# Performance work log

Hardware: AMD Instinct MI355X
Metric: run time of the kernel (lower is better)

Reference implementation:

```python
import jax, jax.numpy as jnp
import numpy as np

IN_DIM = 128
OUT_DIM = 128
NUM_HEADS = 4
HEAD_DIM = OUT_DIM // NUM_HEADS  # 32
B, N = 4, 4096


def setup_inputs() -> dict:
    key = jax.random.key(0)
    ks = jax.random.split(key, 7)
    s_in = 1.0 / np.sqrt(IN_DIM)
    s_out = 1.0 / np.sqrt(OUT_DIM)
    return {
        "x": jax.random.normal(ks[0], (B, N, IN_DIM), dtype=jnp.float32),
        "adjacency": jax.random.randint(ks[1], (N, N), 0, 2, dtype=jnp.int32),
        "W_q": jax.random.uniform(ks[2], (IN_DIM, NUM_HEADS * HEAD_DIM), jnp.float32, -s_in, s_in),
        "W_k": jax.random.uniform(ks[3], (IN_DIM, NUM_HEADS * HEAD_DIM), jnp.float32, -s_in, s_in),
        "W_v": jax.random.uniform(ks[4], (IN_DIM, NUM_HEADS * HEAD_DIM), jnp.float32, -s_in, s_in),
        "W_o": jax.random.uniform(ks[5], (OUT_DIM, OUT_DIM), jnp.float32, -s_out, s_out),
        "b_o": jax.random.uniform(ks[6], (OUT_DIM,), jnp.float32, -s_out, s_out),
    }


def reference(x, adjacency, W_q, W_k, W_v, W_o, b_o):
    Bn, Nn, _ = x.shape
    # QKV projections -> (B, H, N, Dh)
    q = (x @ W_q).reshape(Bn, Nn, NUM_HEADS, HEAD_DIM).transpose(0, 2, 1, 3)
    k = (x @ W_k).reshape(Bn, Nn, NUM_HEADS, HEAD_DIM).transpose(0, 2, 1, 3)
    v = (x @ W_v).reshape(Bn, Nn, NUM_HEADS, HEAD_DIM).transpose(0, 2, 1, 3)
    scores = jnp.einsum("bhnd,bhmd->bhnm", q, k) / np.sqrt(HEAD_DIM).astype(np.float32)
    # adjacency mask (1,1,N,N): -inf where no edge
    adj = adjacency[None, None, :, :]
    scores = jnp.where(adj == 0, -jnp.inf, scores)
    attn = jax.nn.softmax(scores, axis=-1)
    out = jnp.einsum("bhnm,bhmd->bhnd", attn, v)
    out = out.transpose(0, 2, 1, 3).reshape(Bn, Nn, NUM_HEADS * HEAD_DIM)  # concat heads
    return out @ W_o + b_o
```

## Files before the change

### kernel.cpp

```cpp
#include <hip/hip_runtime.h>
#include <stdint.h>

typedef __attribute__((ext_vector_type(4))) short short4v;
typedef __attribute__((ext_vector_type(8))) short bf16x8;
typedef __attribute__((ext_vector_type(4))) float f32x4;
typedef __attribute__((ext_vector_type(2))) uint32_t uint2v;
typedef __attribute__((ext_vector_type(4))) uint32_t uint4v;
typedef __attribute__((ext_vector_type(4))) uint16_t ushort4v;

#define NN 4096

__device__ __forceinline__ uint16_t f2bf(float f) {
    union { float f; uint32_t u; } c; c.f = f;
    uint32_t r = c.u + 0x7FFF + ((c.u >> 16) & 1);
    return (uint16_t)(r >> 16);
}

__global__ __launch_bounds__(256) void pack_kernel(
    const int* __restrict__ adj, uint64_t* __restrict__ bits,
    const float* __restrict__ Wq, const float* __restrict__ Wk,
    const float* __restrict__ Wv, const float* __restrict__ Wo,
    uint16_t* __restrict__ WT, uint16_t* __restrict__ WoT)
{
    const int lane = threadIdx.x & 63;
    const int wave = (blockIdx.x * blockDim.x + threadIdx.x) >> 6;
    const int nwaves = (gridDim.x * blockDim.x) >> 6;
    const int TOT = (NN * NN) / 64;
    for (int i = wave; i < TOT; i += nwaves) {
        int v = adj[(size_t)i * 64 + lane];
        uint64_t m = __ballot(v != 0);
        if (lane == 0) bits[i] = m;
    }
    const int tid = blockIdx.x * blockDim.x + threadIdx.x;
    const int nth = gridDim.x * blockDim.x;
    for (int t = tid; t < 3 * 128 * 128 + 128 * 128; t += nth) {
        if (t < 3 * 128 * 128) {
            int j = t >> 7, k = t & 127;
            int m = j >> 7, jj = j & 127;
            const float* W = (m == 0) ? Wq : ((m == 1) ? Wk : Wv);
            float v = W[k * 128 + jj];
            if (m == 0) v *= (0.17677669529663687f * 1.4426950408889634f);
            WT[t] = f2bf(v);
        } else {
            int t2 = t - 3 * 128 * 128;
            int j = t2 >> 7, k = t2 & 127;
            WoT[t2] = f2bf(Wo[k * 128 + j]);
        }
    }
}

__global__ __launch_bounds__(256) void qkv_kernel(
    const float* __restrict__ x, const uint16_t* __restrict__ WT,
    uint16_t* __restrict__ Q, uint16_t* __restrict__ Kf, uint16_t* __restrict__ Vf)
{
    const int wave = threadIdx.x >> 6, lane = threadIdx.x & 63;
    const int g = lane >> 4, l15 = lane & 15;
    const int ntile = blockIdx.x * 4 + wave;
    const int n = ntile * 16 + l15;
    const int b = n >> 12, nn = n & 4095;

    const char* xrow = (const char*)x + (size_t)n * 512;
    bf16x8 xb[4];
#pragma unroll
    for (int ks = 0; ks < 4; ++ks) {
        f32x4 a = *(const f32x4*)(xrow + ks * 128 + g * 16);
        f32x4 c = *(const f32x4*)(xrow + ks * 128 + 64 + g * 16);
        bf16x8 f;
#pragma unroll
        for (int i = 0; i < 4; ++i) { f[i] = (short)f2bf(a[i]); f[4 + i] = (short)f2bf(c[i]); }
        xb[ks] = f;
    }

#pragma unroll 1
    for (int jt = 0; jt < 24; ++jt) {
        const int j0 = jt * 16;
        const bool isV = (j0 >= 256);
        const char* wrow = (const char*)WT + (size_t)(j0 + l15) * 256;
        f32x4 acc = {0.f, 0.f, 0.f, 0.f};
#pragma unroll
        for (int ks = 0; ks < 4; ++ks) {
            short4v a0 = *(const short4v*)(wrow + ks * 64 + g * 8);
            short4v a1 = *(const short4v*)(wrow + ks * 64 + 32 + g * 8);
            bf16x8 af = __builtin_shufflevector(a0, a1, 0, 1, 2, 3, 4, 5, 6, 7);
            acc = isV ? __builtin_amdgcn_mfma_f32_16x16x32_bf16(xb[ks], af, acc, 0, 0, 0)
                      : __builtin_amdgcn_mfma_f32_16x16x32_bf16(af, xb[ks], acc, 0, 0, 0);
        }
        const int m = j0 >> 7;
        const int bh = b * 4 + ((j0 & 127) >> 5);
        const int half = (j0 >> 4) & 1;
        ushort4v st;
#pragma unroll
        for (int r = 0; r < 4; ++r) st[r] = f2bf(acc[r]);
        if (m == 0) {
            const int d0 = (j0 & 31) + g * 4;
            *(ushort4v*)(Q + ((size_t)bh * 4096 + nn) * 32 + d0) = st;
        } else if (m == 1) {
            *(ushort4v*)(Kf + ((size_t)bh << 17) + (ntile & 255) * 512 + lane * 8 + half * 4) = st;
        } else {
            *(ushort4v*)(Vf + ((size_t)bh << 17) + ((ntile & 255) >> 1) * 1024
                         + half * 512 + lane * 8 + ((ntile & 1) << 2)) = st;
        }
    }
}

__global__ __launch_bounds__(512, 2) void attn_kernel(
    const uint16_t* __restrict__ Q, const uint16_t* __restrict__ Kf,
    const uint16_t* __restrict__ Vf, const uint32_t* __restrict__ bits,
    uint16_t* __restrict__ O)
{
    __shared__ f32x4 cmb[4][4][2][64];
    __shared__ float csum[4][4][64];
    const int tid = threadIdx.x;
    const int wave = tid >> 6, lane = tid & 63;
    const int g = lane >> 4, l15 = lane & 15, gsh = g * 4;
    const int blk = blockIdx.x;
    const int bh = ((blk & 7) << 1) | ((blk >> 3) & 1);
    const int qb = blk >> 4;
    const int q0 = qb * 64;

    const char* Kp = (const char*)Kf + ((size_t)bh << 18) + wave * 32768 + lane * 16;
    const char* Vp = (const char*)Vf + ((size_t)bh << 18) + wave * 32768 + lane * 16;
    const uint32_t* ap[4];
#pragma unroll
    for (int qg = 0; qg < 4; ++qg)
        ap[qg] = bits + (size_t)(q0 + qg * 16 + l15) * 128 + wave * 16;

    bf16x8 qf[4];
#pragma unroll
    for (int qg = 0; qg < 4; ++qg) {
        const char* qrow = (const char*)Q + ((size_t)bh * 4096 + q0 + qg * 16 + l15) * 64;
        short4v a0 = *(const short4v*)(qrow + g * 8);
        short4v a1 = *(const short4v*)(qrow + 32 + g * 8);
        qf[qg] = __builtin_shufflevector(a0, a1, 0, 1, 2, 3, 4, 5, 6, 7);
    }

    bf16x8 ones;
#pragma unroll
    for (int i = 0; i < 8; ++i) ones[i] = (short)0x3F80;

    const f32x4 z = {0.f, 0.f, 0.f, 0.f};
    f32x4 o[4][2], sacc[4];
#pragma unroll
    for (int qg = 0; qg < 4; ++qg) { o[qg][0] = z; o[qg][1] = z; sacc[qg] = z; }

#pragma unroll 1
    for (int t = 0; t < 8; ++t) {
        bf16x8 kc[4], vc[4];
#pragma unroll
        for (int j = 0; j < 4; ++j) kc[j] = *(const bf16x8*)(Kp + j * 1024);
#pragma unroll
        for (int i = 0; i < 4; ++i) vc[i] = *(const bf16x8*)(Vp + i * 1024);
        Kp += 4096; Vp += 4096;
        uint2v wc[4];
#pragma unroll
        for (int qg = 0; qg < 4; ++qg) { wc[qg] = *(const uint2v*)ap[qg]; ap[qg] += 2; }

#pragma unroll
        for (int qg = 0; qg < 4; ++qg) {
            f32x4 s[4];
#pragma unroll
            for (int j = 0; j < 4; ++j)
                s[j] = __builtin_amdgcn_mfma_f32_16x16x32_bf16(kc[j], qf[qg], z, 0, 0, 0);
            float p[16];
#pragma unroll
            for (int j = 0; j < 4; ++j) {
                uint32_t wj = wc[qg][j >> 1] >> (((j & 1) << 4) + gsh);
#pragma unroll
                for (int r = 0; r < 4; ++r) {
                    float pv = __builtin_amdgcn_exp2f(s[j][r]);
                    int msk = ((int)(wj << (31 - r))) >> 31;
                    p[j * 4 + r] = __uint_as_float(__float_as_uint(pv) & (uint32_t)msk);
                }
            }
            uint32_t pk[8];
#pragma unroll
            for (int i = 0; i < 8; ++i) {
                uint32_t r_;
                asm("v_cvt_pk_bf16_f32 %0, %1, %2" : "=v"(r_) : "v"(p[2 * i]), "v"(p[2 * i + 1]));
                pk[i] = r_;
            }
            uint4v u0 = {pk[0], pk[1], pk[2], pk[3]};
            uint4v u1 = {pk[4], pk[5], pk[6], pk[7]};
            bf16x8 pf0 = __builtin_bit_cast(bf16x8, u0);
            bf16x8 pf1 = __builtin_bit_cast(bf16x8, u1);
            o[qg][0] = __builtin_amdgcn_mfma_f32_16x16x32_bf16(vc[0], pf0, o[qg][0], 0, 0, 0);
            o[qg][0] = __builtin_amdgcn_mfma_f32_16x16x32_bf16(vc[2], pf1, o[qg][0], 0, 0, 0);
            o[qg][1] = __builtin_amdgcn_mfma_f32_16x16x32_bf16(vc[1], pf0, o[qg][1], 0, 0, 0);
            o[qg][1] = __builtin_amdgcn_mfma_f32_16x16x32_bf16(vc[3], pf1, o[qg][1], 0, 0, 0);
            sacc[qg] = __builtin_amdgcn_mfma_f32_16x16x32_bf16(ones, pf0, sacc[qg], 0, 0, 0);
            sacc[qg] = __builtin_amdgcn_mfma_f32_16x16x32_bf16(ones, pf1, sacc[qg], 0, 0, 0);
        }
    }

    if (wave < 4) {
#pragma unroll
        for (int qg = 0; qg < 4; ++qg) {
            cmb[wave][qg][0][lane] = o[qg][0];
            cmb[wave][qg][1][lane] = o[qg][1];
            csum[wave][qg][lane] = sacc[qg][0];
        }
    }
    __syncthreads();
    if (wave >= 4) {
        const int w2 = wave - 4;
#pragma unroll
        for (int qg = 0; qg < 4; ++qg) {
            cmb[w2][qg][0][lane] += o[qg][0];
            cmb[w2][qg][1][lane] += o[qg][1];
            csum[w2][qg][lane] += sacc[qg][0];
        }
    }
    __syncthreads();
    {
        const int qg = wave & 3, h = wave >> 2;
        f32x4 a = cmb[0][qg][h][lane] + cmb[1][qg][h][lane]
                + cmb[2][qg][h][lane] + cmb[3][qg][h][lane];
        float sd = csum[0][qg][lane] + csum[1][qg][lane]
                 + csum[2][qg][lane] + csum[3][qg][lane];
        const float inv = 1.0f / sd;
        const int q = q0 + qg * 16 + l15;
        uint16_t* orow = O + ((size_t)bh * 4096 + q) * 32;
        ushort4v st;
#pragma unroll
        for (int r = 0; r < 4; ++r) st[r] = f2bf(a[r] * inv);
        *(ushort4v*)(orow + h * 16 + gsh) = st;
    }
}

__global__ __launch_bounds__(256) void proj_kernel(
    const uint16_t* __restrict__ A, const uint16_t* __restrict__ WoT,
    const float* __restrict__ bo, float* __restrict__ out)
{
    const int wave = threadIdx.x >> 6, lane = threadIdx.x & 63;
    const int g = lane >> 4, l15 = lane & 15;
    const int ntile = blockIdx.x * 4 + wave;
    const int n = ntile * 16 + l15;
    const int b = n >> 12, nn = n & 4095;

    bf16x8 bfr[4];
#pragma unroll
    for (int h = 0; h < 4; ++h) {
        const char* arow = (const char*)A + (((size_t)(b * 4 + h)) * 4096 + nn) * 64;
        short4v a0 = *(const short4v*)(arow + g * 8);
        short4v a1 = *(const short4v*)(arow + 32 + g * 8);
        bfr[h] = __builtin_shufflevector(a0, a1, 0, 1, 2, 3, 4, 5, 6, 7);
    }
#pragma unroll 1
    for (int ct = 0; ct < 8; ++ct) {
        const int c0 = ct * 16;
        const char* wrow = (const char*)WoT + (size_t)(c0 + l15) * 256;
        f32x4 acc = {0.f, 0.f, 0.f, 0.f};
#pragma unroll
        for (int h = 0; h < 4; ++h) {
            short4v a0 = *(const short4v*)(wrow + h * 64 + g * 8);
            short4v a1 = *(const short4v*)(wrow + h * 64 + 32 + g * 8);
            bf16x8 af = __builtin_shufflevector(a0, a1, 0, 1, 2, 3, 4, 5, 6, 7);
            acc = __builtin_amdgcn_mfma_f32_16x16x32_bf16(af, bfr[h], acc, 0, 0, 0);
        }
        f32x4 bias = *(const f32x4*)(bo + c0 + g * 4);
#pragma unroll
        for (int r = 0; r < 4; ++r) acc[r] += bias[r];
        *(f32x4*)(out + (size_t)n * 128 + c0 + g * 4) = acc;
    }
}

extern "C" void kernel_launch(void* const* d_in, const int* in_sizes, int n_in,
                              void* d_out, int out_size, void* d_ws, size_t ws_size,
                              hipStream_t stream)
{
    const float* x   = (const float*)d_in[0];
    const int*   adj = (const int*)d_in[1];
    const float* Wq  = (const float*)d_in[2];
    const float* Wk  = (const float*)d_in[3];
    const float* Wv  = (const float*)d_in[4];
    const float* Wo  = (const float*)d_in[5];
    const float* bo  = (const float*)d_in[6];
    float* out = (float*)d_out;

    char* ws = (char*)d_ws;
    uint16_t* Q    = (uint16_t*)(ws);
    uint16_t* Kf   = (uint16_t*)(ws + ((size_t)4 << 20));
    uint16_t* Vf   = (uint16_t*)(ws + ((size_t)8 << 20));
    uint16_t* AO   = (uint16_t*)(ws + ((size_t)12 << 20));
    uint32_t* bits = (uint32_t*)(ws + ((size_t)16 << 20));
    uint16_t* WT   = (uint16_t*)(ws + ((size_t)18 << 20));
    uint16_t* WoT  = (uint16_t*)(ws + ((size_t)18 << 20) + 98304);

    hipLaunchKernelGGL(pack_kernel, dim3(2048), dim3(256), 0, stream,
                       adj, (uint64_t*)bits, Wq, Wk, Wv, Wo, WT, WoT);
    hipLaunchKernelGGL(qkv_kernel, dim3(256), dim3(256), 0, stream,
                       x, WT, Q, Kf, Vf);
    hipLaunchKernelGGL(attn_kernel, dim3(1024), dim3(512), 0, stream,
                       Q, Kf, Vf, bits, AO);
    hipLaunchKernelGGL(proj_kernel, dim3(256), dim3(256), 0, stream,
                       AO, WoT, bo, out);
}
```

Baseline: 133.2 us.

## Rebalance kernels: split weight pack, overlap adjacency packing with QKV, retile attention

New measurement: 130.1 us. -2.3%, faster.

```diff
diff --git a/kernel.cpp b/kernel.cpp
--- a/kernel.cpp
+++ b/kernel.cpp
@@ -16,46 +16,50 @@
     return (uint16_t)(r >> 16);
 }
 
-__global__ __launch_bounds__(256) void pack_kernel(
-    const int* __restrict__ adj, uint64_t* __restrict__ bits,
+__global__ __launch_bounds__(256) void wpack_kernel(
     const float* __restrict__ Wq, const float* __restrict__ Wk,
     const float* __restrict__ Wv, const float* __restrict__ Wo,
     uint16_t* __restrict__ WT, uint16_t* __restrict__ WoT)
 {
-    const int lane = threadIdx.x & 63;
-    const int wave = (blockIdx.x * blockDim.x + threadIdx.x) >> 6;
-    const int nwaves = (gridDim.x * blockDim.x) >> 6;
-    const int TOT = (NN * NN) / 64;
-    for (int i = wave; i < TOT; i += nwaves) {
-        int v = adj[(size_t)i * 64 + lane];
-        uint64_t m = __ballot(v != 0);
-        if (lane == 0) bits[i] = m;
-    }
-    const int tid = blockIdx.x * blockDim.x + threadIdx.x;
-    const int nth = gridDim.x * blockDim.x;
-    for (int t = tid; t < 3 * 128 * 128 + 128 * 128; t += nth) {
-        if (t < 3 * 128 * 128) {
-            int j = t >> 7, k = t & 127;
-            int m = j >> 7, jj = j & 127;
-            const float* W = (m == 0) ? Wq : ((m == 1) ? Wk : Wv);
-            float v = W[k * 128 + jj];
-            if (m == 0) v *= (0.17677669529663687f * 1.4426950408889634f);
-            WT[t] = f2bf(v);
-        } else {
-            int t2 = t - 3 * 128 * 128;
-            int j = t2 >> 7, k = t2 & 127;
-            WoT[t2] = f2bf(Wo[k * 128 + j]);
-        }
-    }
-}
-
-__global__ __launch_bounds__(256) void qkv_kernel(
+    const int t = blockIdx.x * 256 + threadIdx.x;
+    if (t < 3 * 128 * 128) {
+        int j = t >> 7, k = t & 127;
+        int m = j >> 7, jj = j & 127;
+        const float* W = (m == 0) ? Wq : ((m == 1) ? Wk : Wv);
+        float v = W[k * 128 + jj];
+        if (m == 0) v *= (0.17677669529663687f * 1.4426950408889634f);
+        WT[t] = f2bf(v);
+    } else {
+        int t2 = t - 3 * 128 * 128;
+        int j = t2 >> 7, k = t2 & 127;
+        WoT[t2] = f2bf(Wo[k * 128 + j]);
+    }
+}
+
+__global__ __launch_bounds__(256) void adjqkv_kernel(
+    const int* __restrict__ adj, uint64_t* __restrict__ bits,
     const float* __restrict__ x, const uint16_t* __restrict__ WT,
     uint16_t* __restrict__ Q, uint16_t* __restrict__ Kf, uint16_t* __restrict__ Vf)
 {
-    const int wave = threadIdx.x >> 6, lane = threadIdx.x & 63;
+    const int blk = blockIdx.x;
+    const int tid = threadIdx.x;
+    const int wave = tid >> 6, lane = tid & 63;
+
+    if (blk >= 768) {
+        const int ablk = blk - 768;
+        const int wid = (ablk * 256 + tid) >> 6;
+        const int TOT = (NN * NN) / 64;
+        for (int i = wid; i < TOT; i += 8192) {
+            int v = adj[(size_t)i * 64 + lane];
+            uint64_t m = __ballot(v != 0);
+            if (lane == 0) bits[i] = m;
+        }
+        return;
+    }
+
     const int g = lane >> 4, l15 = lane & 15;
-    const int ntile = blockIdx.x * 4 + wave;
+    const int m = blk >> 8;
+    const int ntile = (blk & 255) * 4 + wave;
     const int n = ntile * 16 + l15;
     const int b = n >> 12, nn = n & 4095;
 
@@ -72,9 +76,9 @@
     }
 
 #pragma unroll 1
-    for (int jt = 0; jt < 24; ++jt) {
+    for (int jt = m * 8; jt < m * 8 + 8; ++jt) {
         const int j0 = jt * 16;
-        const bool isV = (j0 >= 256);
+        const bool isV = (m == 2);
         const char* wrow = (const char*)WT + (size_t)(j0 + l15) * 256;
         f32x4 acc = {0.f, 0.f, 0.f, 0.f};
 #pragma unroll
@@ -85,7 +89,6 @@
             acc = isV ? __builtin_amdgcn_mfma_f32_16x16x32_bf16(xb[ks], af, acc, 0, 0, 0)
                       : __builtin_amdgcn_mfma_f32_16x16x32_bf16(af, xb[ks], acc, 0, 0, 0);
         }
-        const int m = j0 >> 7;
         const int bh = b * 4 + ((j0 & 127) >> 5);
         const int half = (j0 >> 4) & 1;
         ushort4v st;
@@ -103,31 +106,29 @@
     }
 }
 
-__global__ __launch_bounds__(512, 2) void attn_kernel(
+__global__ __launch_bounds__(256) void attn_kernel(
     const uint16_t* __restrict__ Q, const uint16_t* __restrict__ Kf,
     const uint16_t* __restrict__ Vf, const uint32_t* __restrict__ bits,
     uint16_t* __restrict__ O)
 {
-    __shared__ f32x4 cmb[4][4][2][64];
-    __shared__ float csum[4][4][64];
+    __shared__ f32x4 cmb[4][2][2][64];
+    __shared__ float csum[4][2][64];
     const int tid = threadIdx.x;
     const int wave = tid >> 6, lane = tid & 63;
     const int g = lane >> 4, l15 = lane & 15, gsh = g * 4;
     const int blk = blockIdx.x;
     const int bh = ((blk & 7) << 1) | ((blk >> 3) & 1);
     const int qb = blk >> 4;
-    const int q0 = qb * 64;
-
-    const char* Kp = (const char*)Kf + ((size_t)bh << 18) + wave * 32768 + lane * 16;
-    const char* Vp = (const char*)Vf + ((size_t)bh << 18) + wave * 32768 + lane * 16;
-    const uint32_t* ap[4];
-#pragma unroll
-    for (int qg = 0; qg < 4; ++qg)
-        ap[qg] = bits + (size_t)(q0 + qg * 16 + l15) * 128 + wave * 16;
-
-    bf16x8 qf[4];
-#pragma unroll
-    for (int qg = 0; qg < 4; ++qg) {
+    const int q0 = qb * 32;
+
+    const char* Kp = (const char*)Kf + ((size_t)bh << 18) + wave * 65536 + lane * 16;
+    const char* Vp = (const char*)Vf + ((size_t)bh << 18) + wave * 65536 + lane * 16;
+    const uint32_t* ap0 = bits + (size_t)(q0 + l15) * 128 + wave * 32;
+    const uint32_t* ap1 = bits + (size_t)(q0 + 16 + l15) * 128 + wave * 32;
+
+    bf16x8 qf[2];
+#pragma unroll
+    for (int qg = 0; qg < 2; ++qg) {
         const char* qrow = (const char*)Q + ((size_t)bh * 4096 + q0 + qg * 16 + l15) * 64;
         short4v a0 = *(const short4v*)(qrow + g * 8);
         short4v a1 = *(const short4v*)(qrow + 32 + g * 8);
@@ -139,80 +140,65 @@
     for (int i = 0; i < 8; ++i) ones[i] = (short)0x3F80;
 
     const f32x4 z = {0.f, 0.f, 0.f, 0.f};
-    f32x4 o[4][2], sacc[4];
-#pragma unroll
-    for (int qg = 0; qg < 4; ++qg) { o[qg][0] = z; o[qg][1] = z; sacc[qg] = z; }
+    f32x4 o[2][2], sacc[2];
+#pragma unroll
+    for (int qg = 0; qg < 2; ++qg) { o[qg][0] = z; o[qg][1] = z; sacc[qg] = z; }
 
 #pragma unroll 1
-    for (int t = 0; t < 8; ++t) {
+    for (int t = 0; t < 16; ++t) {
         bf16x8 kc[4], vc[4];
 #pragma unroll
         for (int j = 0; j < 4; ++j) kc[j] = *(const bf16x8*)(Kp + j * 1024);
 #pragma unroll
         for (int i = 0; i < 4; ++i) vc[i] = *(const bf16x8*)(Vp + i * 1024);
         Kp += 4096; Vp += 4096;
-        uint2v wc[4];
-#pragma unroll
-        for (int qg = 0; qg < 4; ++qg) { wc[qg] = *(const uint2v*)ap[qg]; ap[qg] += 2; }
-
-#pragma unroll
-        for (int qg = 0; qg < 4; ++qg) {
-            f32x4 s[4];
-#pragma unroll
-            for (int j = 0; j < 4; ++j)
-                s[j] = __builtin_amdgcn_mfma_f32_16x16x32_bf16(kc[j], qf[qg], z, 0, 0, 0);
-            float p[16];
-#pragma unroll
-            for (int j = 0; j < 4; ++j) {
-                uint32_t wj = wc[qg][j >> 1] >> (((j & 1) << 4) + gsh);
+        uint2v wc0 = *(const uint2v*)ap0;  ap0 += 2;
+        uint2v wc1 = *(const uint2v*)ap1;  ap1 += 2;
+
+#pragma unroll
+        for (int qg = 0; qg < 2; ++qg) {
+            const uint2v wc = qg ? wc1 : wc0;
+#pragma unroll
+            for (int half32 = 0; half32 < 2; ++half32) {
+                f32x4 s0 = __builtin_amdgcn_mfma_f32_16x16x32_bf16(kc[half32 * 2], qf[qg], z, 0, 0, 0);
+                f32x4 s1 = __builtin_amdgcn_mfma_f32_16x16x32_bf16(kc[half32 * 2 + 1], qf[qg], z, 0, 0, 0);
+                uint32_t wlo = (wc[half32]) >> gsh;
+                uint32_t whi = (wc[half32]) >> (16 + gsh);
+                float p[8];
 #pragma unroll
                 for (int r = 0; r < 4; ++r) {
-                    float pv = __builtin_amdgcn_exp2f(s[j][r]);
-                    int msk = ((int)(wj << (31 - r))) >> 31;
-                    p[j * 4 + r] = __uint_as_float(__float_as_uint(pv) & (uint32_t)msk);
+                    float pv0 = __builtin_amdgcn_exp2f(s0[r]);
+                    int m0 = ((int)(wlo << (31 - r))) >> 31;
+                    p[r] = __uint_as_float(__float_as_uint(pv0) & (uint32_t)m0);
+                    float pv1 = __builtin_amdgcn_exp2f(s1[r]);
+                    int m1 = ((int)(whi << (31 - r))) >> 31;
+                    p[4 + r] = __uint_as_float(__float_as_uint(pv1) & (uint32_t)m1);
                 }
+                uint32_t pk[4];
+#pragma unroll
+                for (int i = 0; i < 4; ++i) {
+                    uint32_t r_;
+                    asm("v_cvt_pk_bf16_f32 %0, %1, %2" : "=v"(r_) : "v"(p[2 * i]), "v"(p[2 * i + 1]));
+                    pk[i] = r_;
+                }
+                uint4v u = {pk[0], pk[1], pk[2], pk[3]};
+                bf16x8 pf = __builtin_bit_cast(bf16x8, u);
+                o[qg][0] = __builtin_amdgcn_mfma_f32_16x16x32_bf16(vc[half32 * 2], pf, o[qg][0], 0, 0, 0);
+                o[qg][1] = __builtin_amdgcn_mfma_f32_16x16x32_bf16(vc[half32 * 2 + 1], pf, o[qg][1], 0, 0, 0);
+                sacc[qg] = __builtin_amdgcn_mfma_f32_16x16x32_bf16(ones, pf, sacc[qg], 0, 0, 0);
             }
-            uint32_t pk[8];
-#pragma unroll
-            for (int i = 0; i < 8; ++i) {
-                uint32_t r_;
-                asm("v_cvt_pk_bf16_f32 %0, %1, %2" : "=v"(r_) : "v"(p[2 * i]), "v"(p[2 * i + 1]));
-                pk[i] = r_;
-            }
-            uint4v u0 = {pk[0], pk[1], pk[2], pk[3]};
-            uint4v u1 = {pk[4], pk[5], pk[6], pk[7]};
-            bf16x8 pf0 = __builtin_bit_cast(bf16x8, u0);
-            bf16x8 pf1 = __builtin_bit_cast(bf16x8, u1);
-            o[qg][0] = __builtin_amdgcn_mfma_f32_16x16x32_bf16(vc[0], pf0, o[qg][0], 0, 0, 0);
-            o[qg][0] = __builtin_amdgcn_mfma_f32_16x16x32_bf16(vc[2], pf1, o[qg][0], 0, 0, 0);
-            o[qg][1] = __builtin_amdgcn_mfma_f32_16x16x32_bf16(vc[1], pf0, o[qg][1], 0, 0, 0);
-            o[qg][1] = __builtin_amdgcn_mfma_f32_16x16x32_bf16(vc[3], pf1, o[qg][1], 0, 0, 0);
-            sacc[qg] = __builtin_amdgcn_mfma_f32_16x16x32_bf16(ones, pf0, sacc[qg], 0, 0, 0);
-            sacc[qg] = __builtin_amdgcn_mfma_f32_16x16x32_bf16(ones, pf1, sacc[qg], 0, 0, 0);
-        }
-    }
-
-    if (wave < 4) {
-#pragma unroll
-        for (int qg = 0; qg < 4; ++qg) {
-            cmb[wave][qg][0][lane] = o[qg][0];
-            cmb[wave][qg][1][lane] = o[qg][1];
-            csum[wave][qg][lane] = sacc[qg][0];
-        }
-    }
-    __syncthreads();
-    if (wave >= 4) {
-        const int w2 = wave - 4;
-#pragma unroll
-        for (int qg = 0; qg < 4; ++qg) {
-            cmb[w2][qg][0][lane] += o[qg][0];
-            cmb[w2][qg][1][lane] += o[qg][1];
-            csum[w2][qg][lane] += sacc[qg][0];
-        }
+        }
+    }
+
+#pragma unroll
+    for (int qg = 0; qg < 2; ++qg) {
+        cmb[wave][qg][0][lane] = o[qg][0];
+        cmb[wave][qg][1][lane] = o[qg][1];
+        csum[wave][qg][lane] = sacc[qg][0];
     }
     __syncthreads();
     {
-        const int qg = wave & 3, h = wave >> 2;
+        const int qg = wave >> 1, h = wave & 1;
         f32x4 a = cmb[0][qg][h][lane] + cmb[1][qg][h][lane]
                 + cmb[2][qg][h][lane] + cmb[3][qg][h][lane];
         float sd = csum[0][qg][lane] + csum[1][qg][lane]
@@ -233,7 +219,9 @@
 {
     const int wave = threadIdx.x >> 6, lane = threadIdx.x & 63;
     const int g = lane >> 4, l15 = lane & 15;
-    const int ntile = blockIdx.x * 4 + wave;
+    const int blk = blockIdx.x;
+    const int ctbase = (blk >> 8) * 4;
+    const int ntile = (blk & 255) * 4 + wave;
     const int n = ntile * 16 + l15;
     const int b = n >> 12, nn = n & 4095;
 
@@ -246,7 +234,7 @@
         bfr[h] = __builtin_shufflevector(a0, a1, 0, 1, 2, 3, 4, 5, 6, 7);
     }
 #pragma unroll 1
-    for (int ct = 0; ct < 8; ++ct) {
+    for (int ct = ctbase; ct < ctbase + 4; ++ct) {
         const int c0 = ct * 16;
         const char* wrow = (const char*)WoT + (size_t)(c0 + l15) * 256;
         f32x4 acc = {0.f, 0.f, 0.f, 0.f};
@@ -286,12 +274,12 @@
     uint16_t* WT   = (uint16_t*)(ws + ((size_t)18 << 20));
     uint16_t* WoT  = (uint16_t*)(ws + ((size_t)18 << 20) + 98304);
 
-    hipLaunchKernelGGL(pack_kernel, dim3(2048), dim3(256), 0, stream,
-                       adj, (uint64_t*)bits, Wq, Wk, Wv, Wo, WT, WoT);
-    hipLaunchKernelGGL(qkv_kernel, dim3(256), dim3(256), 0, stream,
-                       x, WT, Q, Kf, Vf);
-    hipLaunchKernelGGL(attn_kernel, dim3(1024), dim3(512), 0, stream,
+    hipLaunchKernelGGL(wpack_kernel, dim3(256), dim3(256), 0, stream,
+                       Wq, Wk, Wv, Wo, WT, WoT);
+    hipLaunchKernelGGL(adjqkv_kernel, dim3(2816), dim3(256), 0, stream,
+                       adj, (uint64_t*)bits, x, WT, Q, Kf, Vf);
+    hipLaunchKernelGGL(attn_kernel, dim3(2048), dim3(256), 0, stream,
                        Q, Kf, Vf, bits, AO);
-    hipLaunchKernelGGL(proj_kernel, dim3(256), dim3(256), 0, stream,
+    hipLaunchKernelGGL(proj_kernel, dim3(512), dim3(256), 0, stream,
                        AO, WoT, bo, out);
 }
```
